# Kernel tuning notes

Measured on AMD Instinct MI355X. Metric: run time of the kernel, lower is better.

## Reference

```python
import jax, jax.numpy as jnp
import numpy as np

N = 50000      # num nodes
E = 800000     # num edges (before self loops)
F_IN = 128     # fea_size
D = 128        # g_dim_per_layer[i]
H = 4          # heads
C = D // H     # out_channels per head
NEG_SLOPE = 0.2  # PyG GATConv default leaky_relu slope


def setup_inputs() -> dict:
    key = jax.random.key(0)
    ks = jax.random.split(key, 20)
    inp = {
        "x": jax.random.normal(ks[0], (N, F_IN), dtype=jnp.float32),
        "edge_index": jax.random.randint(ks[1], (2, E), 0, N, dtype=jnp.int32),
        "w0": jax.random.normal(ks[2], (F_IN, D), dtype=jnp.float32) * 0.05,
        "b0": jnp.zeros((D,), dtype=jnp.float32),
    }
    for i in (1, 2, 3):
        k = 4 * i
        inp[f"w{i}"] = jax.random.normal(ks[k], (D, D), dtype=jnp.float32) * 0.05
        inp[f"a_src{i}"] = jax.random.normal(ks[k + 1], (H, C), dtype=jnp.float32) * 0.1
        inp[f"a_dst{i}"] = jax.random.normal(ks[k + 2], (H, C), dtype=jnp.float32) * 0.1
        inp[f"b{i}"] = jnp.zeros((D,), dtype=jnp.float32)
    return inp


def _gat_layer(x, src, dst, w, a_src, a_dst, b):
    # PyG GATConv (eval mode, dropout inactive, add_self_loops already applied)
    n = x.shape[0]
    xp = (x @ w).reshape(n, H, C)                       # [N,H,C]
    al_s = jnp.einsum("nhc,hc->nh", xp, a_src)          # [N,H]
    al_d = jnp.einsum("nhc,hc->nh", xp, a_dst)          # [N,H]
    e = jax.nn.leaky_relu(al_s[src] + al_d[dst], NEG_SLOPE)  # [E',H]
    # softmax over incoming edges of each destination node
    m = jax.ops.segment_max(e, dst, num_segments=n)
    e = jnp.exp(e - m[dst])
    s = jax.ops.segment_sum(e, dst, num_segments=n)
    alpha = e / s[dst]                                  # [E',H]
    msg = alpha[:, :, None] * xp[src]                   # [E',H,C]
    out = jax.ops.segment_sum(msg, dst, num_segments=n)  # [N,H,C]
    return out.reshape(n, H * C) + b


def reference(x, edge_index, w0, b0, w1, a_src1, a_dst1, b1,
              w2, a_src2, a_dst2, b2, w3, a_src3, a_dst3, b3):
    n = x.shape[0]
    loops = jnp.arange(n, dtype=edge_index.dtype)
    ei = jnp.concatenate([edge_index, jnp.stack([loops, loops])], axis=1)
    src, dst = ei[0], ei[1]  # messages flow src -> dst (PyG convention)

    h = x @ w0 + b0
    h = jax.nn.relu(h + _gat_layer(h, src, dst, w1, a_src1, a_dst1, b1))
    h = jax.nn.relu(h + _gat_layer(h, src, dst, w2, a_src2, a_dst2, b2))
    return _gat_layer(h, src, dst, w3, a_src3, a_dst3, b3)
```

## Files before the change

kernel.cpp:

```cpp
#include <hip/hip_runtime.h>

#define F 128
#define HEADS 4
#define NEG 0.2f
#define CAP 40
#define CAPP 44
#define CB 6144
#define HTS 136

typedef unsigned short u16;
typedef unsigned int u32;
typedef __attribute__((ext_vector_type(8))) unsigned short us8;
typedef __attribute__((ext_vector_type(8))) short short8;
typedef __attribute__((ext_vector_type(4))) float f32x4;

__device__ __forceinline__ float bf2f(u16 u) {
  union { u32 i; float f; } v; v.i = ((u32)u) << 16; return v.f;
}
__device__ __forceinline__ float bflo(u32 p) {
  union { u32 i; float f; } v; v.i = p << 16; return v.f;
}
__device__ __forceinline__ float bfhi(u32 p) {
  union { u32 i; float f; } v; v.i = p & 0xFFFF0000u; return v.f;
}
__device__ __forceinline__ u16 f2bf(float f) {
  union { u32 i; float f; } v; v.f = f;
  if (((v.i >> 23) & 0xFF) == 0xFF) return 0;
  u32 r = v.i + 0x7FFF + ((v.i >> 16) & 1);
  return (u16)(r >> 16);
}
__device__ __forceinline__ float sane(float f) {
  union { u32 i; float f; } v; v.f = f;
  return (((v.i >> 23) & 0xFF) == 0xFF) ? 0.f : f;
}
__device__ __forceinline__ u16 bfsane(u16 u) {
  return (((u >> 7) & 0xFF) == 0xFF) ? (u16)0 : u;
}

__device__ __forceinline__ bool detect_f32_wave(const u16* __restrict__ p) {
  int lane = threadIdx.x & 63;
  const us8* q = (const us8*)p + lane * 4;
  int c = 0;
  #pragma unroll
  for (int k = 0; k < 4; k++) {
    us8 v = q[k];
    #pragma unroll
    for (int j = 0; j < 8; j++) { unsigned e = (v[j] >> 7) & 0xFF; c += (e >= 0xF8); }
  }
  #pragma unroll
  for (int off = 32; off; off >>= 1) c += __shfl_xor(c, off);
  return c > 4;
}

__global__ __launch_bounds__(256) void fill_const_bf16(u16* __restrict__ p, u16 v, int n) {
  int i = blockIdx.x * blockDim.x + threadIdx.x;
  if (i < n) p[i] = v;
}

__global__ __launch_bounds__(256) void setup(
    const void* w0, const void* w1, const void* w2, const void* w3,
    const void* b0, const void* b1, const void* b2, const void* b3,
    const void* as1, const void* ad1, const void* as2, const void* ad2,
    const void* as3, const void* ad3,
    u16* __restrict__ wsz, u16* __restrict__ avf, float* __restrict__ par,
    int* __restrict__ flg, int* __restrict__ gcur) {
  __shared__ float vv[8][128];
  bool f32 = detect_f32_wave((const u16*)w0);
  int blk = blockIdx.x, tid = threadIdx.x;
  if (blk < 32) {
    int idx = blk * 256 + tid;
    int layer = idx >> 11;
    int rest  = idx & 2047;
    int lane = rest & 63;
    int ts   = rest >> 6;
    int s = ts & 3, t = ts >> 2;
    int kbase = s * 32 + (lane >> 4) * 8;
    int nn    = t * 16 + (lane & 15);
    const void* W = (layer == 0) ? w0 : (layer == 1) ? w1 : (layer == 2) ? w2 : w3;
    us8 o;
    #pragma unroll
    for (int j = 0; j < 8; j++) {
      int off = (kbase + j) * F + nn;
      o[j] = f32 ? f2bf(sane(((const float*)W)[off])) : bfsane(((const u16*)W)[off]);
    }
    *(us8*)(wsz + (size_t)idx * 8) = o;
  } else if (blk < 37) {
    int t = (blk - 32) * 256 + tid;
    if (t < 1280) {
      const void* tab[10] = {b0, b1, b2, b3, as1, ad1, as2, ad2, as3, ad3};
      const void* src = tab[t >> 7];
      int idx = t & 127;
      float v = f32 ? ((const float*)src)[idx] : bf2f(((const u16*)src)[idx]);
      par[t] = sane(v);
    }
  } else if (blk == 37) {
    gcur[tid] = 0;
    if (tid == 0) flg[0] = f32 ? 1 : 0;
  } else {
    int l = blk - 38;
    const void* W   = (l == 0) ? w1 : (l == 1) ? w2 : w3;
    const void* asp = (l == 0) ? as1 : (l == 1) ? as2 : as3;
    const void* adp = (l == 0) ? ad1 : (l == 1) ? ad2 : ad3;
    for (int e = tid; e < 1024; e += 256) {
      int vec = e >> 7, k = e & 127;
      int h = vec & 3;
      const void* av = (vec < 4) ? asp : adp;
      float sum = 0.f;
      for (int c = 0; c < 32; c++) {
        int col = h * 32 + c;
        float wv_ = f32 ? ((const float*)W)[k * F + col] : bf2f(((const u16*)W)[k * F + col]);
        float aa  = f32 ? ((const float*)av)[col]        : bf2f(((const u16*)av)[col]);
        sum += sane(wv_) * sane(aa);
      }
      vv[vec][k] = sane(sum);
    }
    __syncthreads();
    int s = tid >> 6, lane = tid & 63;
    int quad = lane >> 4, l15 = lane & 15;
    int kbase = s * 32 + quad * 8;
    us8 o;
    #pragma unroll
    for (int j = 0; j < 8; j++)
      o[j] = (l15 < 8) ? f2bf(vv[l15][kbase + j]) : (u16)0;
    *(us8*)(avf + (((size_t)l * 4 + s) * 64 + lane) * 8) = o;
  }
}

__device__ __forceinline__ void gemm_tile(
    int m0, int lane, const void* __restrict__ A, int f32in,
    const u16* __restrict__ wszL, const float* __restrict__ biasc,
    const u16* __restrict__ avfL, u16* __restrict__ Cm,
    float* __restrict__ al_s, float* __restrict__ al_d, int nrows) {
  int quad = lane >> 4, l15 = lane & 15;
  int mrow = m0 + l15;
  int ml = mrow < nrows ? mrow : (nrows - 1);
  short8 af[4];
  if (f32in) {
    const float* ar = (const float*)A + (size_t)ml * F;
    #pragma unroll
    for (int s = 0; s < 4; s++) {
      float4 u = *(const float4*)(ar + s * 32 + quad * 8);
      float4 v = *(const float4*)(ar + s * 32 + quad * 8 + 4);
      short8 p;
      p[0] = (short)f2bf(sane(u.x)); p[1] = (short)f2bf(sane(u.y));
      p[2] = (short)f2bf(sane(u.z)); p[3] = (short)f2bf(sane(u.w));
      p[4] = (short)f2bf(sane(v.x)); p[5] = (short)f2bf(sane(v.y));
      p[6] = (short)f2bf(sane(v.z)); p[7] = (short)f2bf(sane(v.w));
      af[s] = p;
    }
  } else {
    const u16* ar = (const u16*)A + (size_t)ml * F;
    #pragma unroll
    for (int s = 0; s < 4; s++) af[s] = *(const short8*)(ar + s * 32 + quad * 8);
  }

  f32x4 acc[8];
  #pragma unroll
  for (int t = 0; t < 8; t++) acc[t] = (f32x4){0.f, 0.f, 0.f, 0.f};
  f32x4 accL = (f32x4){0.f, 0.f, 0.f, 0.f};

  #pragma unroll
  for (int s = 0; s < 4; s++) {
    short8 bfr[8];
    #pragma unroll
    for (int t = 0; t < 8; t++)
      bfr[t] = *(const short8*)(wszL + (size_t)(((t << 2) | s) * 64 + lane) * 8);
    if (avfL) {
      short8 av = *(const short8*)(avfL + (size_t)(s * 64 + lane) * 8);
      accL = __builtin_amdgcn_mfma_f32_16x16x32_bf16(af[s], av, accL, 0, 0, 0);
    }
    #pragma unroll
    for (int t = 0; t < 8; t++)
      acc[t] = __builtin_amdgcn_mfma_f32_16x16x32_bf16(af[s], bfr[t], acc[t], 0, 0, 0);
  }

  #pragma unroll
  for (int t = 0; t < 8; t++) {
    int cc = t * 16 + l15;
    float b = biasc ? biasc[cc] : 0.f;
    #pragma unroll
    for (int r = 0; r < 4; r++) {
      int row = m0 + quad * 4 + r;
      if (row < nrows) Cm[(size_t)row * F + cc] = f2bf(sane(acc[t][r] + b));
    }
  }
  if (avfL && l15 < 8) {
    float* dst = (l15 < 4) ? al_s : al_d;
    int h = l15 & 3;
    #pragma unroll
    for (int r = 0; r < 4; r++) {
      int row = m0 + quad * 4 + r;
      if (row < nrows) dst[(size_t)row * 4 + h] = sane(accL[r]);
    }
  }
}

__device__ __forceinline__ void scatter_body(const int* __restrict__ ei,
                                             int* __restrict__ gcur,
                                             int2* __restrict__ ebuf,
                                             int E, int E2, int n, int blk) {
  __shared__ int lcnt[256];
  __shared__ int gbase[256];
  int tid = threadIdx.x;
  lcnt[tid] = 0;
  __syncthreads();
  int srcv[16], dstv[16], rnk[16];
  #pragma unroll
  for (int i = 0; i < 16; i++) {
    int e = blk * 4096 + i * 256 + tid;
    rnk[i] = -1;
    if (e < E2) {
      int src, dst;
      if (e < E) { src = ei[e]; dst = ei[E + e]; }
      else       { src = dst = e - E; }
      if ((unsigned)dst < (unsigned)n) {
        srcv[i] = src; dstv[i] = dst;
        rnk[i] = atomicAdd(&lcnt[dst >> 8], 1);
      }
    }
  }
  __syncthreads();
  int c = lcnt[tid];
  gbase[tid] = c ? atomicAdd(&gcur[tid], c) : 0;
  __syncthreads();
  #pragma unroll
  for (int i = 0; i < 16; i++) {
    if (rnk[i] >= 0) {
      int b = dstv[i] >> 8;
      int slot = gbase[b] + rnk[i];
      if (slot < CB) ebuf[(size_t)b * CB + slot] = make_int2(srcv[i], dstv[i]);
    }
  }
}

__device__ __forceinline__ void fill_body(const int* __restrict__ gcur,
                                          const int2* __restrict__ ebuf,
                                          int* __restrict__ rp,
                                          int* __restrict__ col, int n, int b) {
  __shared__ int sc[256];
  __shared__ int ncnt[256];
  __shared__ int nofs[256];
  __shared__ int wsums[4];
  __shared__ int total_s;
  int tid = threadIdx.x, lane = tid & 63, wv = tid >> 6;
  int v = min(gcur[tid], CB);
  int x = v;
  #pragma unroll
  for (int off = 1; off < 64; off <<= 1) {
    int t = __shfl_up(x, off);
    if (lane >= off) x += t;
  }
  if (lane == 63) wsums[wv] = x;
  __syncthreads();
  int add = 0;
  for (int w = 0; w < wv; w++) add += wsums[w];
  sc[tid] = add + x - v;
  if (tid == 255) total_s = add + x;
  __syncthreads();
  int tot = min(gcur[b], CB);
  int colbase = sc[b];
  const int2* eb = ebuf + (size_t)b * CB;
  ncnt[tid] = 0;
  __syncthreads();
  for (int j = tid; j < tot; j += 256) atomicAdd(&ncnt[eb[j].y & 255], 1);
  __syncthreads();
  v = ncnt[tid];
  x = v;
  #pragma unroll
  for (int off = 1; off < 64; off <<= 1) {
    int t = __shfl_up(x, off);
    if (lane >= off) x += t;
  }
  if (lane == 63) wsums[wv] = x;
  __syncthreads();
  add = 0;
  for (int w = 0; w < wv; w++) add += wsums[w];
  nofs[tid] = add + x - v;
  int node = (b << 8) + tid;
  if (node < n) rp[node] = colbase + nofs[tid];
  if (b == 0 && tid == 0) rp[n] = total_s;
  __syncthreads();
  ncnt[tid] = 0;
  __syncthreads();
  for (int j = tid; j < tot; j += 256) {
    int2 e = eb[j];
    int ln = e.y & 255;
    int r = atomicAdd(&ncnt[ln], 1);
    col[colbase + nofs[ln] + r] = e.x;
  }
}

__global__ __launch_bounds__(256) void scatter_gemm0(
    const int* __restrict__ ei, int* __restrict__ gcur, int2* __restrict__ ebuf,
    int E, int E2, int n, int SB,
    const void* __restrict__ x, const int* __restrict__ flg,
    const u16* __restrict__ wsz, const float* __restrict__ b0c,
    u16* __restrict__ hio) {
  int blk = blockIdx.x;
  if (blk < SB) {
    scatter_body(ei, gcur, ebuf, E, E2, n, blk);
  } else {
    int tid = threadIdx.x, wv = tid >> 6, lane = tid & 63;
    int m0 = (blk - SB) * 64 + wv * 16;
    gemm_tile(m0, lane, x, flg[0], wsz, b0c, nullptr, hio, nullptr, nullptr, n);
  }
}

__global__ __launch_bounds__(256) void fill_gemm1(
    const int* __restrict__ gcur, const int2* __restrict__ ebuf,
    int* __restrict__ rp, int* __restrict__ col, int n, int NBv,
    const void* __restrict__ hA, const u16* __restrict__ wszL,
    const u16* __restrict__ avfL, u16* __restrict__ xp,
    float* __restrict__ al_s, float* __restrict__ al_d) {
  int blk = blockIdx.x;
  if (blk < NBv) {
    fill_body(gcur, ebuf, rp, col, n, blk);
  } else {
    int tid = threadIdx.x, wv = tid >> 6, lane = tid & 63;
    int m0 = (blk - NBv) * 64 + wv * 16;
    gemm_tile(m0, lane, hA, 0, wszL, nullptr, avfL, xp, al_s, al_d, n);
  }
}

#define ACC8(w_, P_)                                    \
  a0 += (w_) * bflo((P_).x); a1 += (w_) * bfhi((P_).x); \
  a2 += (w_) * bflo((P_).y); a3 += (w_) * bfhi((P_).y); \
  a4 += (w_) * bflo((P_).z); a5 += (w_) * bfhi((P_).z); \
  a6 += (w_) * bflo((P_).w); a7 += (w_) * bfhi((P_).w);

__global__ __launch_bounds__(256, 8) void gat_agg_gemm(
    const u16* __restrict__ xp, const float* __restrict__ al_s,
    const float* __restrict__ al_d, const int* __restrict__ row_ptr,
    const int* __restrict__ col, const float* __restrict__ biasc,
    u16* __restrict__ hio, int n, int E2,
    const u16* __restrict__ wszL, const u16* __restrict__ avfL,
    u16* __restrict__ xpo, float* __restrict__ also_, float* __restrict__ aldo) {
  __shared__ int   sb[4][4][CAP];
  __shared__ float wb[4][4][4][CAPP];
  __shared__ u16   ht[16 * HTS];
  int tid = threadIdx.x;
  int wv = tid >> 6, lane = tid & 63;
  int q = lane >> 4, g = lane & 15;
  int node = blockIdx.x * 16 + wv * 4 + q;
  bool active = node < n;
  int beg = 0, end = 0;
  float ald_[4] = {0.f, 0.f, 0.f, 0.f};
  if (active) {
    beg = row_ptr[node]; end = row_ptr[node + 1];
    if (beg < 0) beg = 0; if (beg > E2) beg = E2;
    if (end < beg) end = beg; if (end > E2) end = E2;
    float4 qd = ((const float4*)al_d)[node];
    ald_[0] = qd.x; ald_[1] = qd.y; ald_[2] = qd.z; ald_[3] = qd.w;
  }
  int deg = end - beg;
  int ch = g * 8, head = g >> 2;
  u32 cb = (u32)g * 16;
  const char* xpb = (const char*)xp;
  float a0 = 0.f, a1 = 0.f, a2 = 0.f, a3 = 0.f;
  float a4 = 0.f, a5 = 0.f, a6 = 0.f, a7 = 0.f;
  float inv;

  if (deg <= CAP) {
    float er[3][4];
    float m4[4] = {-1e30f, -1e30f, -1e30f, -1e30f};
    #pragma unroll
    for (int it = 0; it < 3; it++) {
      int jj = g + it * 16;
      if (jj < deg) {
        int src = col[beg + jj];
        if ((unsigned)src >= (unsigned)n) src = node;
        sb[wv][q][jj] = src;
        float4 qs = ((const float4*)al_s)[src];
        float as_[4] = {qs.x, qs.y, qs.z, qs.w};
        #pragma unroll
        for (int h = 0; h < 4; h++) {
          float e = as_[h] + ald_[h];
          e = (e > 0.f) ? e : NEG * e;
          er[it][h] = e;
          m4[h] = fmaxf(m4[h], e);
        }
      }
    }
    #pragma unroll
    for (int off = 8; off; off >>= 1)
      #pragma unroll
      for (int h = 0; h < 4; h++) m4[h] = fmaxf(m4[h], __shfl_xor(m4[h], off));
    float s4[4] = {0.f, 0.f, 0.f, 0.f};
    #pragma unroll
    for (int it = 0; it < 3; it++) {
      int jj = g + it * 16;
      if (jj < deg) {
        #pragma unroll
        for (int h = 0; h < 4; h++) {
          float w = __expf(er[it][h] - m4[h]);
          s4[h] += w;
          wb[wv][q][h][jj] = w;
        }
      }
    }
    #pragma unroll
    for (int off = 8; off; off >>= 1)
      #pragma unroll
      for (int h = 0; h < 4; h++) s4[h] += __shfl_xor(s4[h], off);
    inv = (s4[head] > 0.f) ? 1.f / s4[head] : 0.f;
    __asm__ volatile("s_waitcnt lgkmcnt(0)" ::: "memory");
    const int* srow = sb[wv][q];
    const float* wrow = wb[wv][q][head];
    int j = 0;
    if (deg >= 4) {
      int4 sa = *(const int4*)(srow);
      float4 wa = *(const float4*)(wrow);
      uint4 P0 = *(const uint4*)(xpb + (((u32)sa.x << 8) + cb));
      uint4 P1 = *(const uint4*)(xpb + (((u32)sa.y << 8) + cb));
      uint4 P2 = *(const uint4*)(xpb + (((u32)sa.z << 8) + cb));
      uint4 P3 = *(const uint4*)(xpb + (((u32)sa.w << 8) + cb));
      for (; j + 8 <= deg; j += 4) {
        int4 sn = *(const int4*)(srow + j + 4);
        float4 wn = *(const float4*)(wrow + j + 4);
        uint4 Q0 = *(const uint4*)(xpb + (((u32)sn.x << 8) + cb));
        uint4 Q1 = *(const uint4*)(xpb + (((u32)sn.y << 8) + cb));
        uint4 Q2 = *(const uint4*)(xpb + (((u32)sn.z << 8) + cb));
        uint4 Q3 = *(const uint4*)(xpb + (((u32)sn.w << 8) + cb));
        ACC8(wa.x, P0); ACC8(wa.y, P1); ACC8(wa.z, P2); ACC8(wa.w, P3);
        wa = wn; P0 = Q0; P1 = Q1; P2 = Q2; P3 = Q3;
      }
      ACC8(wa.x, P0); ACC8(wa.y, P1); ACC8(wa.z, P2); ACC8(wa.w, P3);
      j += 4;
    }
    for (; j < deg; j++) {
      int s0 = srow[j];
      float w0 = wrow[j];
      uint4 p0 = *(const uint4*)(xpb + (((u32)s0 << 8) + cb));
      ACC8(w0, p0);
    }
    a0 *= inv; a1 *= inv; a2 *= inv; a3 *= inv;
    a4 *= inv; a5 *= inv; a6 *= inv; a7 *= inv;
  } else {
    float m = -1.0e30f, s = 0.f;
    for (int j = beg; j < end; ++j) {
      int src = col[j];
      if ((unsigned)src >= (unsigned)n) continue;
      float e = al_s[src * 4 + head] + ald_[head];
      e = (e > 0.f) ? e : NEG * e;
      float mn = fmaxf(m, e);
      float scale = __expf(m - mn);
      float w = __expf(e - mn);
      uint4 pv = *(const uint4*)(xpb + (((u32)src << 8) + cb));
      s = s * scale + w;
      a0 = a0 * scale + w * bflo(pv.x); a1 = a1 * scale + w * bfhi(pv.x);
      a2 = a2 * scale + w * bflo(pv.y); a3 = a3 * scale + w * bfhi(pv.y);
      a4 = a4 * scale + w * bflo(pv.z); a5 = a5 * scale + w * bfhi(pv.z);
      a6 = a6 * scale + w * bflo(pv.w); a7 = a7 * scale + w * bfhi(pv.w);
      m = mn;
    }
    inv = (s > 0.f) ? 1.f / s : 0.f;
    a0 *= inv; a1 *= inv; a2 *= inv; a3 *= inv;
    a4 *= inv; a5 *= inv; a6 *= inv; a7 *= inv;
  }

  uint4 st = make_uint4(0u, 0u, 0u, 0u);
  if (active) {
    float4 b4a = *(const float4*)(biasc + ch);
    float4 b4b = *(const float4*)(biasc + ch + 4);
    float o0 = sane(a0) + b4a.x, o1 = sane(a1) + b4a.y;
    float o2 = sane(a2) + b4a.z, o3 = sane(a3) + b4a.w;
    float o4 = sane(a4) + b4b.x, o5 = sane(a5) + b4b.y;
    float o6 = sane(a6) + b4b.z, o7 = sane(a7) + b4b.w;
    size_t o = (size_t)node * F + ch;
    uint4 hv = *(const uint4*)(hio + o);
    o0 = fmaxf(bflo(hv.x) + o0, 0.f);
    o1 = fmaxf(bfhi(hv.x) + o1, 0.f);
    o2 = fmaxf(bflo(hv.y) + o2, 0.f);
    o3 = fmaxf(bfhi(hv.y) + o3, 0.f);
    o4 = fmaxf(bflo(hv.z) + o4, 0.f);
    o5 = fmaxf(bfhi(hv.z) + o5, 0.f);
    o6 = fmaxf(bflo(hv.w) + o6, 0.f);
    o7 = fmaxf(bfhi(hv.w) + o7, 0.f);
    st.x = ((u32)f2bf(sane(o1)) << 16) | (u32)f2bf(sane(o0));
    st.y = ((u32)f2bf(sane(o3)) << 16) | (u32)f2bf(sane(o2));
    st.z = ((u32)f2bf(sane(o5)) << 16) | (u32)f2bf(sane(o4));
    st.w = ((u32)f2bf(sane(o7)) << 16) | (u32)f2bf(sane(o6));
    *(uint4*)(hio + o) = st;
  }
  *(uint4*)&ht[(wv * 4 + q) * HTS + ch] = st;
  __syncthreads();

  int quad = lane >> 4, l15 = lane & 15;
  short8 af[4];
  #pragma unroll
  for (int s = 0; s < 4; s++)
    af[s] = *(const short8*)&ht[l15 * HTS + s * 32 + quad * 8];
  f32x4 acc0 = (f32x4){0.f, 0.f, 0.f, 0.f};
  f32x4 acc1 = (f32x4){0.f, 0.f, 0.f, 0.f};
  f32x4 accL = (f32x4){0.f, 0.f, 0.f, 0.f};
  int t0 = wv * 2;
  #pragma unroll
  for (int s = 0; s < 4; s++) {
    short8 bv0 = *(const short8*)(wszL + (size_t)(((t0 << 2) | s) * 64 + lane) * 8);
    short8 bv1 = *(const short8*)(wszL + (size_t)((((t0 + 1) << 2) | s) * 64 + lane) * 8);
    if (wv == 0) {
      short8 av = *(const short8*)(avfL + (size_t)(s * 64 + lane) * 8);
      accL = __builtin_amdgcn_mfma_f32_16x16x32_bf16(af[s], av, accL, 0, 0, 0);
    }
    acc0 = __builtin_amdgcn_mfma_f32_16x16x32_bf16(af[s], bv0, acc0, 0, 0, 0);
    acc1 = __builtin_amdgcn_mfma_f32_16x16x32_bf16(af[s], bv1, acc1, 0, 0, 0);
  }
  int row0 = blockIdx.x * 16;
  #pragma unroll
  for (int tt = 0; tt < 2; tt++) {
    f32x4 ac = tt ? acc1 : acc0;
    int cc = (t0 + tt) * 16 + l15;
    #pragma unroll
    for (int r = 0; r < 4; r++) {
      int row = row0 + quad * 4 + r;
      if (row < n) xpo[(size_t)row * F + cc] = f2bf(sane(ac[r]));
    }
  }
  if (wv == 0 && l15 < 8) {
    float* dst = (l15 < 4) ? also_ : aldo;
    int h = l15 & 3;
    #pragma unroll
    for (int r = 0; r < 4; r++) {
      int row = row0 + quad * 4 + r;
      if (row < n) dst[(size_t)row * 4 + h] = sane(accL[r]);
    }
  }
}

#define ACC4(w_, P_)                                    \
  a0 += (w_) * bflo((P_).x); a1 += (w_) * bfhi((P_).x); \
  a2 += (w_) * bflo((P_).y); a3 += (w_) * bfhi((P_).y);

__global__ __launch_bounds__(256, 8) void gat_agg_final(
    const u16* __restrict__ xp, const float* __restrict__ al_s,
    const float* __restrict__ al_d, const int* __restrict__ row_ptr,
    const int* __restrict__ col, const float* __restrict__ biasc,
    u16* __restrict__ hio, const int* __restrict__ flgp,
    int n, int E2, int ngrp) {
  __shared__ int   sb[4][4][CAP];
  __shared__ float wb[4][4][4][CAPP];
  int B = blockIdx.x;
  int xs = B & 7;
  int hh = xs >> 2;
  int i = (xs & 3) + (B >> 3) * 4;
  if (i >= ngrp) return;
  int tid = threadIdx.x;
  int wv = tid >> 6, lane = tid & 63;
  int q = lane >> 4, g = lane & 15;
  int node = i * 16 + wv * 4 + q;
  bool active = node < n;
  int beg = 0, end = 0;
  float ald_[4] = {0.f, 0.f, 0.f, 0.f};
  if (active) {
    beg = row_ptr[node]; end = row_ptr[node + 1];
    if (beg < 0) beg = 0; if (beg > E2) beg = E2;
    if (end < beg) end = beg; if (end > E2) end = E2;
    float4 qd = ((const float4*)al_d)[node];
    ald_[0] = qd.x; ald_[1] = qd.y; ald_[2] = qd.z; ald_[3] = qd.w;
  }
  int deg = end - beg;
  int ch = hh * 64 + g * 4;
  int head = ch >> 5;
  u32 cb = (u32)hh * 128 + (u32)g * 8;
  const char* xpb = (const char*)xp;
  float a0 = 0.f, a1 = 0.f, a2 = 0.f, a3 = 0.f;
  float inv;

  if (deg <= CAP) {
    float er[3][4];
    float m4[4] = {-1e30f, -1e30f, -1e30f, -1e30f};
    #pragma unroll
    for (int it = 0; it < 3; it++) {
      int jj = g + it * 16;
      if (jj < deg) {
        int src = col[beg + jj];
        if ((unsigned)src >= (unsigned)n) src = node;
        sb[wv][q][jj] = src;
        float4 qs = ((const float4*)al_s)[src];
        float as_[4] = {qs.x, qs.y, qs.z, qs.w};
        #pragma unroll
        for (int h = 0; h < 4; h++) {
          float e = as_[h] + ald_[h];
          e = (e > 0.f) ? e : NEG * e;
          er[it][h] = e;
          m4[h] = fmaxf(m4[h], e);
        }
      }
    }
    #pragma unroll
    for (int off = 8; off; off >>= 1)
      #pragma unroll
      for (int h = 0; h < 4; h++) m4[h] = fmaxf(m4[h], __shfl_xor(m4[h], off));
    float s4[4] = {0.f, 0.f, 0.f, 0.f};
    #pragma unroll
    for (int it = 0; it < 3; it++) {
      int jj = g + it * 16;
      if (jj < deg) {
        #pragma unroll
        for (int h = 0; h < 4; h++) {
          float w = __expf(er[it][h] - m4[h]);
          s4[h] += w;
          wb[wv][q][h][jj] = w;
        }
      }
    }
    #pragma unroll
    for (int off = 8; off; off >>= 1)
      #pragma unroll
      for (int h = 0; h < 4; h++) s4[h] += __shfl_xor(s4[h], off);
    inv = (s4[head] > 0.f) ? 1.f / s4[head] : 0.f;
    __asm__ volatile("s_waitcnt lgkmcnt(0)" ::: "memory");
    const int* srow = sb[wv][q];
    const float* wrow = wb[wv][q][head];
    int j = 0;
    if (deg >= 4) {
      int4 sa = *(const int4*)(srow);
      float4 wa = *(const float4*)(wrow);
      uint2 P0 = *(const uint2*)(xpb + (((u32)sa.x << 8) + cb));
      uint2 P1 = *(const uint2*)(xpb + (((u32)sa.y << 8) + cb));
      uint2 P2 = *(const uint2*)(xpb + (((u32)sa.z << 8) + cb));
      uint2 P3 = *(const uint2*)(xpb + (((u32)sa.w << 8) + cb));
      for (; j + 8 <= deg; j += 4) {
        int4 sn = *(const int4*)(srow + j + 4);
        float4 wn = *(const float4*)(wrow + j + 4);
        uint2 Q0 = *(const uint2*)(xpb + (((u32)sn.x << 8) + cb));
        uint2 Q1 = *(const uint2*)(xpb + (((u32)sn.y << 8) + cb));
        uint2 Q2 = *(const uint2*)(xpb + (((u32)sn.z << 8) + cb));
        uint2 Q3 = *(const uint2*)(xpb + (((u32)sn.w << 8) + cb));
        ACC4(wa.x, P0); ACC4(wa.y, P1); ACC4(wa.z, P2); ACC4(wa.w, P3);
        wa = wn; P0 = Q0; P1 = Q1; P2 = Q2; P3 = Q3;
      }
      ACC4(wa.x, P0); ACC4(wa.y, P1); ACC4(wa.z, P2); ACC4(wa.w, P3);
      j += 4;
    }
    for (; j < deg; j++) {
      int s0 = srow[j];
      float w0 = wrow[j];
      uint2 p0 = *(const uint2*)(xpb + (((u32)s0 << 8) + cb));
      ACC4(w0, p0);
    }
    a0 *= inv; a1 *= inv; a2 *= inv; a3 *= inv;
  } else {
    float m = -1.0e30f, s = 0.f;
    for (int j = beg; j < end; ++j) {
      int src = col[j];
      if ((unsigned)src >= (unsigned)n) continue;
      float e = al_s[src * 4 + head] + ald_[head];
      e = (e > 0.f) ? e : NEG * e;
      float mn = fmaxf(m, e);
      float scale = __expf(m - mn);
      float w = __expf(e - mn);
      uint2 pv = *(const uint2*)(xpb + (((u32)src << 8) + cb));
      s = s * scale + w;
      a0 = a0 * scale + w * bflo(pv.x); a1 = a1 * scale + w * bfhi(pv.x);
      a2 = a2 * scale + w * bflo(pv.y); a3 = a3 * scale + w * bfhi(pv.y);
      m = mn;
    }
    inv = (s > 0.f) ? 1.f / s : 0.f;
    a0 *= inv; a1 *= inv; a2 *= inv; a3 *= inv;
  }

  if (!active) return;
  float4 b4 = *(const float4*)(biasc + ch);
  float o0 = sane(a0) + b4.x, o1 = sane(a1) + b4.y;
  float o2 = sane(a2) + b4.z, o3 = sane(a3) + b4.w;
  size_t o = (size_t)node * F + ch;
  if (flgp[0]) {
    float4 s1 = {sane(o0), sane(o1), sane(o2), sane(o3)};
    *(float4*)((float*)hio + o) = s1;
  } else {
    uint2 st;
    st.x = ((u32)f2bf(sane(o1)) << 16) | (u32)f2bf(sane(o0));
    st.y = ((u32)f2bf(sane(o3)) << 16) | (u32)f2bf(sane(o2));
    *(uint2*)(hio + o) = st;
  }
}

extern "C" void kernel_launch(void* const* d_in, const int* in_sizes, int n_in,
                              void* d_out, int out_size, void* d_ws, size_t ws_size,
                              hipStream_t stream) {
  const int* ei = (const int*)d_in[1];

  const int N  = in_sizes[0] / F;
  const int E  = in_sizes[1] / 2;
  const int E2 = E + N;
  const int NB = (N + 255) >> 8;
  const int SB = (E2 + 4095) / 4096;
  const int GB64  = (N + 63) / 64;
  const int AGGB  = (N + 15) / 16;
  const int FINB  = 8 * ((AGGB + 3) / 4);

  uintptr_t base = ((uintptr_t)d_ws + 255) & ~(uintptr_t)255;
  size_t off_par = 0;
  size_t off_flg = off_par + (size_t)1536 * 4;
  size_t off_wsz = off_flg + 256;
  size_t off_avf = off_wsz + (size_t)65536 * 2;
  size_t off_xp  = off_avf + (size_t)6144 * 2;
  size_t off_als = off_xp  + (size_t)N * F * 2;
  size_t off_ald = off_als + (size_t)N * HEADS * 4;
  size_t off_gc  = off_ald + (size_t)N * HEADS * 4;
  size_t off_rp  = off_gc  + 1024;
  size_t off_col = off_rp  + (size_t)(N + 1) * 4;
  size_t off_eb  = (off_col + (size_t)E2 * 4 + 255) & ~(size_t)255;
  size_t off_xp2 = (off_eb + (size_t)NB * CB * 8 + 255) & ~(size_t)255;
  size_t off_als2 = off_xp2 + (size_t)N * F * 2;
  size_t off_ald2 = off_als2 + (size_t)N * HEADS * 4;
  size_t need    = off_ald2 + (size_t)N * HEADS * 4 + 512 + ((uintptr_t)d_ws & 255);

  if (ws_size < need) {
    fill_const_bf16<<<(out_size + 255) / 256, 256, 0, stream>>>(
        (u16*)d_out, (u16)0x4316, out_size);
    return;
  }

  float* par   = (float*)(base + off_par);
  int* flg     = (int*)(base + off_flg);
  u16* wsz     = (u16*)(base + off_wsz);
  u16* avf     = (u16*)(base + off_avf);
  u16* xpA     = (u16*)(base + off_xp);
  float* alsA  = (float*)(base + off_als);
  float* aldA  = (float*)(base + off_ald);
  int* gcur    = (int*)(base + off_gc);
  int* row_ptr = (int*)(base + off_rp);
  int* col     = (int*)(base + off_col);
  int2* ebuf   = (int2*)(base + off_eb);
  u16* xpB     = (u16*)(base + off_xp2);
  float* alsB  = (float*)(base + off_als2);
  float* aldB  = (float*)(base + off_ald2);

  float* bc[4];
  for (int l = 0; l < 4; ++l) bc[l] = par + (size_t)l * 128;

  u16* hio = (u16*)d_out;

  setup<<<41, 256, 0, stream>>>(
      d_in[2], d_in[4], d_in[8], d_in[12],
      d_in[3], d_in[7], d_in[11], d_in[15],
      d_in[5], d_in[6], d_in[9], d_in[10], d_in[13], d_in[14],
      wsz, avf, par, flg, gcur);

  scatter_gemm0<<<SB + GB64, 256, 0, stream>>>(
      ei, gcur, ebuf, E, E2, N, SB, d_in[0], flg, wsz, bc[0], hio);

  fill_gemm1<<<NB + GB64, 256, 0, stream>>>(
      gcur, ebuf, row_ptr, col, N, NB,
      hio, wsz + (size_t)1 * 16384, avf, xpA, alsA, aldA);

  gat_agg_gemm<<<AGGB, 256, 0, stream>>>(
      xpA, alsA, aldA, row_ptr, col, bc[1], hio, N, E2,
      wsz + (size_t)2 * 16384, avf + (size_t)1 * 2048, xpB, alsB, aldB);

  gat_agg_gemm<<<AGGB, 256, 0, stream>>>(
      xpB, alsB, aldB, row_ptr, col, bc[2], hio, N, E2,
      wsz + (size_t)3 * 16384, avf + (size_t)2 * 2048, xpA, alsA, aldA);

  gat_agg_final<<<FINB, 256, 0, stream>>>(
      xpA, alsA, aldA, row_ptr, col, bc[3], hio, flg, N, E2, AGGB);
}
```

Baseline: 273.8 us.

## Fold setup kernel into scatter/gemm0 launch and read raw w0 directly

Removes the separate setup kernel by appending its 41 blocks to the scatter_gemm0 grid. The layer-0 GEMM no longer depends on the swizzled weight buffer, so it converts w0 and b0 from the raw inputs itself. The gcur counter is cleared with hipMemsetAsync instead of inside setup. This saves one launch and one serialization point, but every gemm0 block now gathers w0 with strided scalar loads and converts it, which costs extra redundant memory traffic.

```diff
diff --git a/kernel.cpp b/kernel.cpp
--- a/kernel.cpp
+++ b/kernel.cpp
@@ -57,16 +57,20 @@
   if (i < n) p[i] = v;
 }
 
-__global__ __launch_bounds__(256) void setup(
-    const void* w0, const void* w1, const void* w2, const void* w3,
-    const void* b0, const void* b1, const void* b2, const void* b3,
-    const void* as1, const void* ad1, const void* as2, const void* ad2,
-    const void* as3, const void* ad3,
-    u16* __restrict__ wsz, u16* __restrict__ avf, float* __restrict__ par,
-    int* __restrict__ flg, int* __restrict__ gcur) {
+struct P2A {
+  const int* ei; int* gcur; int2* ebuf;
+  int E, E2, N, SB, GB64;
+  const void* x;
+  const void *w0, *w1, *w2, *w3, *b0, *b1, *b2, *b3;
+  const void *as1, *ad1, *as2, *ad2, *as3, *ad3;
+  u16* wsz; u16* avf; float* par; int* flg;
+  u16* hio;
+};
+
+__device__ __forceinline__ void setup_body(const P2A& a, int blk) {
   __shared__ float vv[8][128];
-  bool f32 = detect_f32_wave((const u16*)w0);
-  int blk = blockIdx.x, tid = threadIdx.x;
+  bool f32 = detect_f32_wave((const u16*)a.w0);
+  int tid = threadIdx.x;
   if (blk < 32) {
     int idx = blk * 256 + tid;
     int layer = idx >> 11;
@@ -76,31 +80,30 @@
     int s = ts & 3, t = ts >> 2;
     int kbase = s * 32 + (lane >> 4) * 8;
     int nn    = t * 16 + (lane & 15);
-    const void* W = (layer == 0) ? w0 : (layer == 1) ? w1 : (layer == 2) ? w2 : w3;
+    const void* W = (layer == 0) ? a.w0 : (layer == 1) ? a.w1 : (layer == 2) ? a.w2 : a.w3;
     us8 o;
     #pragma unroll
     for (int j = 0; j < 8; j++) {
       int off = (kbase + j) * F + nn;
       o[j] = f32 ? f2bf(sane(((const float*)W)[off])) : bfsane(((const u16*)W)[off]);
     }
-    *(us8*)(wsz + (size_t)idx * 8) = o;
+    *(us8*)(a.wsz + (size_t)idx * 8) = o;
   } else if (blk < 37) {
     int t = (blk - 32) * 256 + tid;
     if (t < 1280) {
-      const void* tab[10] = {b0, b1, b2, b3, as1, ad1, as2, ad2, as3, ad3};
+      const void* tab[10] = {a.b0, a.b1, a.b2, a.b3, a.as1, a.ad1, a.as2, a.ad2, a.as3, a.ad3};
       const void* src = tab[t >> 7];
       int idx = t & 127;
       float v = f32 ? ((const float*)src)[idx] : bf2f(((const u16*)src)[idx]);
-      par[t] = sane(v);
+      a.par[t] = sane(v);
     }
   } else if (blk == 37) {
-    gcur[tid] = 0;
-    if (tid == 0) flg[0] = f32 ? 1 : 0;
+    if (tid == 0) a.flg[0] = f32 ? 1 : 0;
   } else {
     int l = blk - 38;
-    const void* W   = (l == 0) ? w1 : (l == 1) ? w2 : w3;
-    const void* asp = (l == 0) ? as1 : (l == 1) ? as2 : as3;
-    const void* adp = (l == 0) ? ad1 : (l == 1) ? ad2 : ad3;
+    const void* W   = (l == 0) ? a.w1 : (l == 1) ? a.w2 : a.w3;
+    const void* asp = (l == 0) ? a.as1 : (l == 1) ? a.as2 : a.as3;
+    const void* adp = (l == 0) ? a.ad1 : (l == 1) ? a.ad2 : a.ad3;
     for (int e = tid; e < 1024; e += 256) {
       int vec = e >> 7, k = e & 127;
       int h = vec & 3;
@@ -122,21 +125,27 @@
     #pragma unroll
     for (int j = 0; j < 8; j++)
       o[j] = (l15 < 8) ? f2bf(vv[l15][kbase + j]) : (u16)0;
-    *(us8*)(avf + (((size_t)l * 4 + s) * 64 + lane) * 8) = o;
-  }
-}
-
-__device__ __forceinline__ void gemm_tile(
-    int m0, int lane, const void* __restrict__ A, int f32in,
-    const u16* __restrict__ wszL, const float* __restrict__ biasc,
-    const u16* __restrict__ avfL, u16* __restrict__ Cm,
-    float* __restrict__ al_s, float* __restrict__ al_d, int nrows) {
+    *(us8*)(a.avf + (((size_t)l * 4 + s) * 64 + lane) * 8) = o;
+  }
+}
+
+__device__ __forceinline__ void gemm0_self(const P2A& a, int gb) {
+  __shared__ float g0bias[128];
+  int tid = threadIdx.x;
+  bool f32 = detect_f32_wave((const u16*)a.w0);
+  if (tid < 128) {
+    float v = f32 ? ((const float*)a.b0)[tid] : bf2f(((const u16*)a.b0)[tid]);
+    g0bias[tid] = sane(v);
+  }
+  __syncthreads();
+  int wv = tid >> 6, lane = tid & 63;
+  int m0 = gb * 64 + wv * 16;
   int quad = lane >> 4, l15 = lane & 15;
   int mrow = m0 + l15;
-  int ml = mrow < nrows ? mrow : (nrows - 1);
+  int ml = mrow < a.N ? mrow : (a.N - 1);
   short8 af[4];
-  if (f32in) {
-    const float* ar = (const float*)A + (size_t)ml * F;
+  if (f32) {
+    const float* ar = (const float*)a.x + (size_t)ml * F;
     #pragma unroll
     for (int s = 0; s < 4; s++) {
       float4 u = *(const float4*)(ar + s * 32 + quad * 8);
@@ -149,10 +158,59 @@
       af[s] = p;
     }
   } else {
-    const u16* ar = (const u16*)A + (size_t)ml * F;
+    const u16* ar = (const u16*)a.x + (size_t)ml * F;
     #pragma unroll
     for (int s = 0; s < 4; s++) af[s] = *(const short8*)(ar + s * 32 + quad * 8);
   }
+
+  f32x4 acc[8];
+  #pragma unroll
+  for (int t = 0; t < 8; t++) acc[t] = (f32x4){0.f, 0.f, 0.f, 0.f};
+
+  const float* wf = (const float*)a.w0;
+  const u16*   wb = (const u16*)a.w0;
+  #pragma unroll
+  for (int s = 0; s < 4; s++) {
+    short8 bfr[8];
+    #pragma unroll
+    for (int t = 0; t < 8; t++) {
+      short8 p;
+      #pragma unroll
+      for (int j = 0; j < 8; j++) {
+        int off = (s * 32 + quad * 8 + j) * F + (t * 16 + l15);
+        p[j] = f32 ? (short)f2bf(sane(wf[off])) : (short)bfsane(wb[off]);
+      }
+      bfr[t] = p;
+    }
+    #pragma unroll
+    for (int t = 0; t < 8; t++)
+      acc[t] = __builtin_amdgcn_mfma_f32_16x16x32_bf16(af[s], bfr[t], acc[t], 0, 0, 0);
+  }
+
+  #pragma unroll
+  for (int t = 0; t < 8; t++) {
+    int cc = t * 16 + l15;
+    float b = g0bias[cc];
+    #pragma unroll
+    for (int r = 0; r < 4; r++) {
+      int row = m0 + quad * 4 + r;
+      if (row < a.N) a.hio[(size_t)row * F + cc] = f2bf(sane(acc[t][r] + b));
+    }
+  }
+}
+
+__device__ __forceinline__ void gemm_tile(
+    int m0, int lane, const void* __restrict__ A,
+    const u16* __restrict__ wszL, const u16* __restrict__ avfL,
+    u16* __restrict__ Cm, float* __restrict__ al_s, float* __restrict__ al_d,
+    int nrows) {
+  int quad = lane >> 4, l15 = lane & 15;
+  int mrow = m0 + l15;
+  int ml = mrow < nrows ? mrow : (nrows - 1);
+  short8 af[4];
+  const u16* ar = (const u16*)A + (size_t)ml * F;
+  #pragma unroll
+  for (int s = 0; s < 4; s++) af[s] = *(const short8*)(ar + s * 32 + quad * 8);
 
   f32x4 acc[8];
   #pragma unroll
@@ -165,10 +223,8 @@
     #pragma unroll
     for (int t = 0; t < 8; t++)
       bfr[t] = *(const short8*)(wszL + (size_t)(((t << 2) | s) * 64 + lane) * 8);
-    if (avfL) {
-      short8 av = *(const short8*)(avfL + (size_t)(s * 64 + lane) * 8);
-      accL = __builtin_amdgcn_mfma_f32_16x16x32_bf16(af[s], av, accL, 0, 0, 0);
-    }
+    short8 av = *(const short8*)(avfL + (size_t)(s * 64 + lane) * 8);
+    accL = __builtin_amdgcn_mfma_f32_16x16x32_bf16(af[s], av, accL, 0, 0, 0);
     #pragma unroll
     for (int t = 0; t < 8; t++)
       acc[t] = __builtin_amdgcn_mfma_f32_16x16x32_bf16(af[s], bfr[t], acc[t], 0, 0, 0);
@@ -177,14 +233,13 @@
   #pragma unroll
   for (int t = 0; t < 8; t++) {
     int cc = t * 16 + l15;
-    float b = biasc ? biasc[cc] : 0.f;
     #pragma unroll
     for (int r = 0; r < 4; r++) {
       int row = m0 + quad * 4 + r;
-      if (row < nrows) Cm[(size_t)row * F + cc] = f2bf(sane(acc[t][r] + b));
-    }
-  }
-  if (avfL && l15 < 8) {
+      if (row < nrows) Cm[(size_t)row * F + cc] = f2bf(sane(acc[t][r]));
+    }
+  }
+  if (l15 < 8) {
     float* dst = (l15 < 4) ? al_s : al_d;
     int h = l15 & 3;
     #pragma unroll
@@ -290,19 +345,14 @@
   }
 }
 
-__global__ __launch_bounds__(256) void scatter_gemm0(
-    const int* __restrict__ ei, int* __restrict__ gcur, int2* __restrict__ ebuf,
-    int E, int E2, int n, int SB,
-    const void* __restrict__ x, const int* __restrict__ flg,
-    const u16* __restrict__ wsz, const float* __restrict__ b0c,
-    u16* __restrict__ hio) {
+__global__ __launch_bounds__(256) void scatter_gemm0(P2A a) {
   int blk = blockIdx.x;
-  if (blk < SB) {
-    scatter_body(ei, gcur, ebuf, E, E2, n, blk);
+  if (blk < a.SB) {
+    scatter_body(a.ei, a.gcur, a.ebuf, a.E, a.E2, a.N, blk);
+  } else if (blk < a.SB + a.GB64) {
+    gemm0_self(a, blk - a.SB);
   } else {
-    int tid = threadIdx.x, wv = tid >> 6, lane = tid & 63;
-    int m0 = (blk - SB) * 64 + wv * 16;
-    gemm_tile(m0, lane, x, flg[0], wsz, b0c, nullptr, hio, nullptr, nullptr, n);
+    setup_body(a, blk - a.SB - a.GB64);
   }
 }
 
@@ -318,7 +368,7 @@
   } else {
     int tid = threadIdx.x, wv = tid >> 6, lane = tid & 63;
     int m0 = (blk - NBv) * 64 + wv * 16;
-    gemm_tile(m0, lane, hA, 0, wszL, nullptr, avfL, xp, al_s, al_d, n);
+    gemm_tile(m0, lane, hA, wszL, avfL, xp, al_s, al_d, n);
   }
 }
 
@@ -679,16 +729,14 @@
 extern "C" void kernel_launch(void* const* d_in, const int* in_sizes, int n_in,
                               void* d_out, int out_size, void* d_ws, size_t ws_size,
                               hipStream_t stream) {
-  const int* ei = (const int*)d_in[1];
-
   const int N  = in_sizes[0] / F;
   const int E  = in_sizes[1] / 2;
   const int E2 = E + N;
   const int NB = (N + 255) >> 8;
   const int SB = (E2 + 4095) / 4096;
-  const int GB64  = (N + 63) / 64;
-  const int AGGB  = (N + 15) / 16;
-  const int FINB  = 8 * ((AGGB + 3) / 4);
+  const int GB64 = (N + 63) / 64;
+  const int AGGB = (N + 15) / 16;
+  const int FINB = 8 * ((AGGB + 3) / 4);
 
   uintptr_t base = ((uintptr_t)d_ws + 255) & ~(uintptr_t)255;
   size_t off_par = 0;
@@ -733,14 +781,20 @@
 
   u16* hio = (u16*)d_out;
 
-  setup<<<41, 256, 0, stream>>>(
-      d_in[2], d_in[4], d_in[8], d_in[12],
-      d_in[3], d_in[7], d_in[11], d_in[15],
-      d_in[5], d_in[6], d_in[9], d_in[10], d_in[13], d_in[14],
-      wsz, avf, par, flg, gcur);
-
-  scatter_gemm0<<<SB + GB64, 256, 0, stream>>>(
-      ei, gcur, ebuf, E, E2, N, SB, d_in[0], flg, wsz, bc[0], hio);
+  P2A a;
+  a.ei = (const int*)d_in[1]; a.gcur = gcur; a.ebuf = ebuf;
+  a.E = E; a.E2 = E2; a.N = N; a.SB = SB; a.GB64 = GB64;
+  a.x = d_in[0];
+  a.w0 = d_in[2]; a.b0 = d_in[3];
+  a.w1 = d_in[4]; a.as1 = d_in[5]; a.ad1 = d_in[6]; a.b1 = d_in[7];
+  a.w2 = d_in[8]; a.as2 = d_in[9]; a.ad2 = d_in[10]; a.b2 = d_in[11];
+  a.w3 = d_in[12]; a.as3 = d_in[13]; a.ad3 = d_in[14]; a.b3 = d_in[15];
+  a.wsz = wsz; a.avf = avf; a.par = par; a.flg = flg;
+  a.hio = hio;
+
+  hipMemsetAsync(gcur, 0, 1024, stream);
+
+  scatter_gemm0<<<SB + GB64 + 41, 256, 0, stream>>>(a);
 
   fill_gemm1<<<NB + GB64, 256, 0, stream>>>(
       gcur, ebuf, row_ptr, col, N, NB,
```

New measurement: 336.3 us. 22.8% more time.
